# Kernel tuning notes

Measured on AMD Instinct MI355X. Metric: run time of the kernel, lower is better.

The kernel has to match this reference:

```python
import jax, jax.numpy as jnp
import numpy as np

SIGMA = 1.0


def _rbf_kernel(X, sigma):
    # pairwise squared Euclidean distances: ||xi||^2 + ||xj||^2 - 2 xi.xj
    sq = jnp.sum(X * X, axis=1)  # [n]
    d2 = sq[:, None] + sq[None, :] - 2.0 * (X @ X.T)
    d2 = jnp.maximum(d2, 0.0)
    return jnp.exp(-d2 / (2.0 * sigma ** 2))


def _center(K):
    # Kc = H @ K @ H with H = I - 11^T/n, done in O(n^2):
    # Kc = K - row_mean - col_mean + grand_mean
    row_mean = jnp.mean(K, axis=1, keepdims=True)   # [n,1]
    col_mean = jnp.mean(K, axis=0, keepdims=True)   # [1,n]
    grand = jnp.mean(K)
    return K - row_mean - col_mean + grand


def setup_inputs() -> dict:
    key = jax.random.key(0)
    k1, k2 = jax.random.split(key)
    X = jax.random.normal(k1, (8192, 512), dtype=jnp.float32)
    Y = jax.random.normal(k2, (8192, 512), dtype=jnp.float32)
    return {"X": X, "Y": Y}


def reference(X, Y):
    n = X.shape[0]
    K = _rbf_kernel(X, SIGMA)
    L = _rbf_kernel(Y, SIGMA)
    Kc = _center(K)
    Lc = _center(L)
    # trace(Kc @ Lc) == sum(Kc * Lc^T) == sum(Kc * Lc) since Lc symmetric
    hsic_value = jnp.sum(Kc * Lc) / (n - 1) ** 2
    return hsic_value
```

## Files before the change

### kernel.cpp

```cpp
#include <hip/hip_runtime.h>
#include <hip/hip_bf16.h>

#define N 8192
#define D 512
#define BM 128
#define BK 64

typedef __attribute__((ext_vector_type(4))) float f32x4;
typedef __attribute__((ext_vector_type(8))) short bf16x8;

__device__ __forceinline__ void g2l16(const void* g, void* l) {
  __builtin_amdgcn_global_load_lds(
      (const __attribute__((address_space(1))) void*)g,
      (__attribute__((address_space(3))) void*)l, 16, 0, 0);
}

__device__ __forceinline__ unsigned short f32_to_bf16(float f) {
  unsigned int u = __float_as_uint(f);
  unsigned int r = (u + 0x7fffu + ((u >> 16) & 1u)) >> 16;
  return (unsigned short)r;
}

__device__ __forceinline__ int lds_off(int row, int kobyte) {
  return row * BK + ((kobyte ^ ((row & 7) << 4)) >> 1);
}

__global__ __launch_bounds__(128) void prep_kernel(
    const float* __restrict__ X, const float* __restrict__ Y,
    unsigned short* __restrict__ Xb, unsigned short* __restrict__ Yb,
    float* __restrict__ sqX, float* __restrict__ sqY) {
  const int b = blockIdx.x;
  const int row = b & (N - 1);
  const float* src = (b < N) ? X : Y;
  unsigned short* dst = (b < N) ? Xb : Yb;
  float* sq = (b < N) ? sqX : sqY;
  const int t = threadIdx.x;
  float4 v = reinterpret_cast<const float4*>(src + (size_t)row * D)[t];
  unsigned short b0 = f32_to_bf16(v.x), b1 = f32_to_bf16(v.y),
                 b2 = f32_to_bf16(v.z), b3 = f32_to_bf16(v.w);
  float f0 = __uint_as_float((unsigned)b0 << 16);
  float f1 = __uint_as_float((unsigned)b1 << 16);
  float f2 = __uint_as_float((unsigned)b2 << 16);
  float f3 = __uint_as_float((unsigned)b3 << 16);
  float s = f0 * f0 + f1 * f1 + f2 * f2 + f3 * f3;
  ushort4 o; o.x = b0; o.y = b1; o.z = b2; o.w = b3;
  reinterpret_cast<ushort4*>(dst + (size_t)row * D)[t] = o;
  #pragma unroll
  for (int msk = 1; msk < 64; msk <<= 1) s += __shfl_xor(s, msk);
  __shared__ float red[2];
  if ((t & 63) == 0) red[t >> 6] = s;
  __syncthreads();
  if (t == 0) sq[row] = red[0] + red[1];
}

__global__ __launch_bounds__(256, 2) void hsic_main(
    const unsigned short* __restrict__ Xb, const unsigned short* __restrict__ Yb,
    const float* __restrict__ sqX, const float* __restrict__ sqY,
    float* __restrict__ rowK, float* __restrict__ rowL,
    float* __restrict__ sums) {
  __shared__ __align__(16) unsigned short sXi[BM * BK];
  __shared__ __align__(16) unsigned short sXj[BM * BK];
  __shared__ __align__(16) unsigned short sYi[BM * BK];
  __shared__ __align__(16) unsigned short sYj[BM * BK];

  const int bid = blockIdx.x;
  int ti = (int)((129.0f - sqrtf(16641.0f - 8.0f * (float)bid)) * 0.5f);
  while (ti > 0 && (ti * (129 - ti)) / 2 > bid) --ti;
  while (((ti + 1) * (128 - ti)) / 2 <= bid) ++ti;
  const int tj = ti + (bid - (ti * (129 - ti)) / 2);
  const bool diag = (ti == tj);

  const int ib = ti * BM, jb = tj * BM;
  const int t = threadIdx.x;
  const int lane = t & 63, wave = t >> 6;
  const int wr = wave >> 1, wc = wave & 1;
  const int fr = lane & 15, fq = lane >> 4;

  f32x4 accK[4][4], accL[4][4];
  #pragma unroll
  for (int m = 0; m < 4; ++m)
    #pragma unroll
    for (int n = 0; n < 4; ++n) { accK[m][n] = (f32x4)0.f; accL[m][n] = (f32x4)0.f; }

  const unsigned short* s0 = Xb + (size_t)ib * D;
  const unsigned short* s1 = Xb + (size_t)jb * D;
  const unsigned short* s2 = Yb + (size_t)ib * D;
  const unsigned short* s3 = Yb + (size_t)jb * D;

  const int srow = t >> 3;
  const int scb = (t & 7) * 16;
  const int swcb = scb ^ ((srow & 7) << 4);

  for (int kt = 0; kt < D / BK; ++kt) {
    const int kb = kt * BK;
    #pragma unroll
    for (int q = 0; q < 4; ++q) {
      const int row = q * 32 + srow;
      const size_t goff = (size_t)row * D + kb + (swcb >> 1);
      const int loff = q * 2048 + t * 8;
      g2l16(s0 + goff, sXi + loff);
      g2l16(s1 + goff, sXj + loff);
      g2l16(s2 + goff, sYi + loff);
      g2l16(s3 + goff, sYj + loff);
    }
    __syncthreads();
    #pragma unroll
    for (int kk = 0; kk < 2; ++kk) {
      const int kob = kk * 64 + fq * 16;
      bf16x8 a[4], b[4];
      #pragma unroll
      for (int m = 0; m < 4; ++m)
        a[m] = *(const bf16x8*)&sXi[lds_off(wr * 64 + m * 16 + fr, kob)];
      #pragma unroll
      for (int n = 0; n < 4; ++n)
        b[n] = *(const bf16x8*)&sXj[lds_off(wc * 64 + n * 16 + fr, kob)];
      #pragma unroll
      for (int m = 0; m < 4; ++m)
        #pragma unroll
        for (int n = 0; n < 4; ++n)
          accK[m][n] = __builtin_amdgcn_mfma_f32_16x16x32_bf16(a[m], b[n], accK[m][n], 0, 0, 0);
      #pragma unroll
      for (int m = 0; m < 4; ++m)
        a[m] = *(const bf16x8*)&sYi[lds_off(wr * 64 + m * 16 + fr, kob)];
      #pragma unroll
      for (int n = 0; n < 4; ++n)
        b[n] = *(const bf16x8*)&sYj[lds_off(wc * 64 + n * 16 + fr, kob)];
      #pragma unroll
      for (int m = 0; m < 4; ++m)
        #pragma unroll
        for (int n = 0; n < 4; ++n)
          accL[m][n] = __builtin_amdgcn_mfma_f32_16x16x32_bf16(a[m], b[n], accL[m][n], 0, 0, 0);
    }
    __syncthreads();
  }

  float sxj[4], syj[4];
  #pragma unroll
  for (int n = 0; n < 4; ++n) {
    const int j = jb + wc * 64 + n * 16 + fr;
    sxj[n] = sqX[j];
    syj[n] = sqY[j];
  }
  float kl = 0.f;
  float ckK[4] = {0.f, 0.f, 0.f, 0.f}, ckL[4] = {0.f, 0.f, 0.f, 0.f};
  #pragma unroll
  for (int m = 0; m < 4; ++m) {
    #pragma unroll
    for (int r = 0; r < 4; ++r) {
      const int i = ib + wr * 64 + m * 16 + fq * 4 + r;
      const float sxi = sqX[i], syi = sqY[i];
      float rk = 0.f, rl = 0.f;
      #pragma unroll
      for (int n = 0; n < 4; ++n) {
        float dK = fmaxf(sxi + sxj[n] - 2.f * accK[m][n][r], 0.f);
        float Kv = __expf(-0.5f * dK);
        float dL = fmaxf(syi + syj[n] - 2.f * accL[m][n][r], 0.f);
        float Lv = __expf(-0.5f * dL);
        kl += Kv * Lv;
        rk += Kv; rl += Lv;
        ckK[n] += Kv; ckL[n] += Lv;
      }
      #pragma unroll
      for (int msk = 1; msk < 16; msk <<= 1) {
        rk += __shfl_xor(rk, msk);
        rl += __shfl_xor(rl, msk);
      }
      if (fr == 0) {
        atomicAdd(&rowK[i], rk);
        atomicAdd(&rowL[i], rl);
      }
    }
  }
  if (!diag) {
    #pragma unroll
    for (int n = 0; n < 4; ++n) {
      float a = ckK[n], b = ckL[n];
      a += __shfl_xor(a, 16); a += __shfl_xor(a, 32);
      b += __shfl_xor(b, 16); b += __shfl_xor(b, 32);
      if (fq == 0) {
        const int j = jb + wc * 64 + n * 16 + fr;
        atomicAdd(&rowK[j], a);
        atomicAdd(&rowL[j], b);
      }
    }
    kl *= 2.f;
  }
  #pragma unroll
  for (int msk = 1; msk < 64; msk <<= 1) kl += __shfl_xor(kl, msk);
  __shared__ float klred[4];
  if (lane == 0) klred[wave] = kl;
  __syncthreads();
  if (t == 0) atomicAdd(sums, klred[0] + klred[1] + klred[2] + klred[3]);
}

__global__ __launch_bounds__(256) void finalize_kernel(
    const float* __restrict__ rowK, const float* __restrict__ rowL,
    const float* __restrict__ sums, float* __restrict__ out) {
  const int t = threadIdx.x;
  float dp = 0.f, sk = 0.f, sl = 0.f;
  for (int i = t; i < N; i += 256) {
    float a = rowK[i], b = rowL[i];
    dp += a * b; sk += a; sl += b;
  }
  #pragma unroll
  for (int msk = 1; msk < 64; msk <<= 1) {
    dp += __shfl_xor(dp, msk);
    sk += __shfl_xor(sk, msk);
    sl += __shfl_xor(sl, msk);
  }
  __shared__ float r[3][4];
  const int wave = t >> 6, lane = t & 63;
  if (lane == 0) { r[0][wave] = dp; r[1][wave] = sk; r[2][wave] = sl; }
  __syncthreads();
  if (t == 0) {
    float DP = r[0][0] + r[0][1] + r[0][2] + r[0][3];
    float SK = r[1][0] + r[1][1] + r[1][2] + r[1][3];
    float SL = r[2][0] + r[2][1] + r[2][2] + r[2][3];
    const float n = (float)N;
    float raw = sums[0] - (2.f / n) * DP + (SK / n) * (SL / n);
    out[0] = raw / ((n - 1.f) * (n - 1.f));
  }
}

extern "C" void kernel_launch(void* const* d_in, const int* in_sizes, int n_in,
                              void* d_out, int out_size, void* d_ws, size_t ws_size,
                              hipStream_t stream) {
  const float* X = (const float*)d_in[0];
  const float* Y = (const float*)d_in[1];
  char* ws = (char*)d_ws;
  unsigned short* Xb = (unsigned short*)ws;
  unsigned short* Yb = (unsigned short*)(ws + (size_t)N * D * 2);
  float* sqX = (float*)(ws + (size_t)N * D * 4);
  float* sqY = sqX + N;
  float* rowK = sqY + N;
  float* rowL = rowK + N;
  float* sums = rowL + N;

  hipMemsetAsync(rowK, 0, (size_t)(2 * N + 16) * sizeof(float), stream);
  prep_kernel<<<2 * N, 128, 0, stream>>>(X, Y, Xb, Yb, sqX, sqY);
  const int ntiles = (N / BM) * (N / BM + 1) / 2;
  hsic_main<<<ntiles, 256, 0, stream>>>(Xb, Yb, sqX, sqY, rowK, rowL, sums);
  finalize_kernel<<<1, 256, 0, stream>>>(rowK, rowL, sums, (float*)d_out);
}
```

Before: 187.7 us.

## Software-pipeline X/Y tile staging so global loads overlap MFMA compute

Splits each K-step into separate X and Y stages. Once an operand's fragments are in registers, the next K-tile for that operand is issued with async global-to-LDS loads, and the MFMAs run while those loads are in flight. Manual vmcnt/lgkmcnt waits and raw barriers replace the two __syncthreads per iteration, and s_setprio raises wave priority around the MFMA blocks. This hides global memory latency without adding LDS, but it holds twice as many fragment registers and relies on hand-counted wait counts being correct.

```diff
diff --git a/kernel.cpp b/kernel.cpp
--- a/kernel.cpp
+++ b/kernel.cpp
@@ -91,7 +91,7 @@
   const int scb = (t & 7) * 16;
   const int swcb = scb ^ ((srow & 7) << 4);
 
-  for (int kt = 0; kt < D / BK; ++kt) {
+  auto stageX = [&](int kt) {
     const int kb = kt * BK;
     #pragma unroll
     for (int q = 0; q < 4; ++q) {
@@ -100,39 +100,71 @@
       const int loff = q * 2048 + t * 8;
       g2l16(s0 + goff, sXi + loff);
       g2l16(s1 + goff, sXj + loff);
+    }
+  };
+  auto stageY = [&](int kt) {
+    const int kb = kt * BK;
+    #pragma unroll
+    for (int q = 0; q < 4; ++q) {
+      const int row = q * 32 + srow;
+      const size_t goff = (size_t)row * D + kb + (swcb >> 1);
+      const int loff = q * 2048 + t * 8;
       g2l16(s2 + goff, sYi + loff);
       g2l16(s3 + goff, sYj + loff);
     }
-    __syncthreads();
+  };
+
+  bf16x8 a[2][4], b[2][4];
+  auto loadFrags = [&](const unsigned short* si, const unsigned short* sj) {
     #pragma unroll
     for (int kk = 0; kk < 2; ++kk) {
       const int kob = kk * 64 + fq * 16;
-      bf16x8 a[4], b[4];
       #pragma unroll
       for (int m = 0; m < 4; ++m)
-        a[m] = *(const bf16x8*)&sXi[lds_off(wr * 64 + m * 16 + fr, kob)];
+        a[kk][m] = *(const bf16x8*)&si[lds_off(wr * 64 + m * 16 + fr, kob)];
       #pragma unroll
       for (int n = 0; n < 4; ++n)
-        b[n] = *(const bf16x8*)&sXj[lds_off(wc * 64 + n * 16 + fr, kob)];
+        b[kk][n] = *(const bf16x8*)&sj[lds_off(wc * 64 + n * 16 + fr, kob)];
+    }
+  };
+  auto mmaInto = [&](f32x4 (&acc)[4][4]) {
+    __builtin_amdgcn_s_setprio(1);
+    #pragma unroll
+    for (int kk = 0; kk < 2; ++kk)
       #pragma unroll
       for (int m = 0; m < 4; ++m)
         #pragma unroll
         for (int n = 0; n < 4; ++n)
-          accK[m][n] = __builtin_amdgcn_mfma_f32_16x16x32_bf16(a[m], b[n], accK[m][n], 0, 0, 0);
-      #pragma unroll
-      for (int m = 0; m < 4; ++m)
-        a[m] = *(const bf16x8*)&sYi[lds_off(wr * 64 + m * 16 + fr, kob)];
-      #pragma unroll
-      for (int n = 0; n < 4; ++n)
-        b[n] = *(const bf16x8*)&sYj[lds_off(wc * 64 + n * 16 + fr, kob)];
-      #pragma unroll
-      for (int m = 0; m < 4; ++m)
-        #pragma unroll
-        for (int n = 0; n < 4; ++n)
-          accL[m][n] = __builtin_amdgcn_mfma_f32_16x16x32_bf16(a[m], b[n], accL[m][n], 0, 0, 0);
-    }
-    __syncthreads();
-  }
+          acc[m][n] = __builtin_amdgcn_mfma_f32_16x16x32_bf16(a[kk][m], b[kk][n], acc[m][n], 0, 0, 0);
+    __builtin_amdgcn_s_setprio(0);
+  };
+
+  stageX(0);
+  stageY(0);
+  for (int kt = 0; kt < 7; ++kt) {
+    asm volatile("s_waitcnt vmcnt(8)" ::: "memory");
+    __builtin_amdgcn_s_barrier();
+    loadFrags(sXi, sXj);
+    asm volatile("s_waitcnt lgkmcnt(0)" ::: "memory");
+    __builtin_amdgcn_s_barrier();
+    stageX(kt + 1);
+    mmaInto(accK);
+    asm volatile("s_waitcnt vmcnt(8)" ::: "memory");
+    __builtin_amdgcn_s_barrier();
+    loadFrags(sYi, sYj);
+    asm volatile("s_waitcnt lgkmcnt(0)" ::: "memory");
+    __builtin_amdgcn_s_barrier();
+    stageY(kt + 1);
+    mmaInto(accL);
+  }
+  asm volatile("s_waitcnt vmcnt(8)" ::: "memory");
+  __builtin_amdgcn_s_barrier();
+  loadFrags(sXi, sXj);
+  mmaInto(accK);
+  asm volatile("s_waitcnt vmcnt(0)" ::: "memory");
+  __builtin_amdgcn_s_barrier();
+  loadFrags(sYi, sYj);
+  mmaInto(accL);
 
   float sxj[4], syj[4];
   #pragma unroll
@@ -174,13 +206,13 @@
   if (!diag) {
     #pragma unroll
     for (int n = 0; n < 4; ++n) {
-      float a = ckK[n], b = ckL[n];
-      a += __shfl_xor(a, 16); a += __shfl_xor(a, 32);
-      b += __shfl_xor(b, 16); b += __shfl_xor(b, 32);
+      float a2 = ckK[n], b2 = ckL[n];
+      a2 += __shfl_xor(a2, 16); a2 += __shfl_xor(a2, 32);
+      b2 += __shfl_xor(b2, 16); b2 += __shfl_xor(b2, 32);
       if (fq == 0) {
         const int j = jb + wc * 64 + n * 16 + fr;
-        atomicAdd(&rowK[j], a);
-        atomicAdd(&rowL[j], b);
+        atomicAdd(&rowK[j], a2);
+        atomicAdd(&rowL[j], b2);
       }
     }
     kl *= 2.f;
```

Result: faster. 175.9 us (-6.3%).

## Load MFMA operands directly from global memory, drop LDS staging, remap blocks for XCDs

Applied to the files above, without the earlier changes.

Removes the shared-memory tiles and barriers: each wave now loads its bf16 A/B fragments straight from global memory (relying on L1/L2 for reuse across waves) and issues the MFMAs, with s_setprio raised around the MFMA burst. The block index is permuted so consecutive tiles are spread across the 8 XCDs (blockIdx&7 chunks of 260), aiming to improve L2 locality. The occupancy hint in launch_bounds is dropped. This trades LDS traffic and sync cost for redundant global/cache loads, since each operand row is fetched by two waves with no LDS sharing, and there is no software prefetch to hide load latency.

```diff
diff --git a/kernel.cpp b/kernel.cpp
--- a/kernel.cpp
+++ b/kernel.cpp
@@ -4,25 +4,15 @@
 #define N 8192
 #define D 512
 #define BM 128
-#define BK 64
+#define NKT 16
 
 typedef __attribute__((ext_vector_type(4))) float f32x4;
 typedef __attribute__((ext_vector_type(8))) short bf16x8;
-
-__device__ __forceinline__ void g2l16(const void* g, void* l) {
-  __builtin_amdgcn_global_load_lds(
-      (const __attribute__((address_space(1))) void*)g,
-      (__attribute__((address_space(3))) void*)l, 16, 0, 0);
-}
 
 __device__ __forceinline__ unsigned short f32_to_bf16(float f) {
   unsigned int u = __float_as_uint(f);
   unsigned int r = (u + 0x7fffu + ((u >> 16) & 1u)) >> 16;
   return (unsigned short)r;
-}
-
-__device__ __forceinline__ int lds_off(int row, int kobyte) {
-  return row * BK + ((kobyte ^ ((row & 7) << 4)) >> 1);
 }
 
 __global__ __launch_bounds__(128) void prep_kernel(
@@ -53,17 +43,12 @@
   if (t == 0) sq[row] = red[0] + red[1];
 }
 
-__global__ __launch_bounds__(256, 2) void hsic_main(
+__global__ __launch_bounds__(256) void hsic_main(
     const unsigned short* __restrict__ Xb, const unsigned short* __restrict__ Yb,
     const float* __restrict__ sqX, const float* __restrict__ sqY,
     float* __restrict__ rowK, float* __restrict__ rowL,
     float* __restrict__ sums) {
-  __shared__ __align__(16) unsigned short sXi[BM * BK];
-  __shared__ __align__(16) unsigned short sXj[BM * BK];
-  __shared__ __align__(16) unsigned short sYi[BM * BK];
-  __shared__ __align__(16) unsigned short sYj[BM * BK];
-
-  const int bid = blockIdx.x;
+  const int bid = (blockIdx.x & 7) * 260 + (blockIdx.x >> 3);
   int ti = (int)((129.0f - sqrtf(16641.0f - 8.0f * (float)bid)) * 0.5f);
   while (ti > 0 && (ti * (129 - ti)) / 2 > bid) --ti;
   while (((ti + 1) * (128 - ti)) / 2 <= bid) ++ti;
@@ -82,56 +67,42 @@
     #pragma unroll
     for (int n = 0; n < 4; ++n) { accK[m][n] = (f32x4)0.f; accL[m][n] = (f32x4)0.f; }
 
-  const unsigned short* s0 = Xb + (size_t)ib * D;
-  const unsigned short* s1 = Xb + (size_t)jb * D;
-  const unsigned short* s2 = Yb + (size_t)ib * D;
-  const unsigned short* s3 = Yb + (size_t)jb * D;
-
-  const int srow = t >> 3;
-  const int scb = (t & 7) * 16;
-  const int swcb = scb ^ ((srow & 7) << 4);
-
-  for (int kt = 0; kt < D / BK; ++kt) {
-    const int kb = kt * BK;
-    #pragma unroll
-    for (int q = 0; q < 4; ++q) {
-      const int row = q * 32 + srow;
-      const size_t goff = (size_t)row * D + kb + (swcb >> 1);
-      const int loff = q * 2048 + t * 8;
-      g2l16(s0 + goff, sXi + loff);
-      g2l16(s1 + goff, sXj + loff);
-      g2l16(s2 + goff, sYi + loff);
-      g2l16(s3 + goff, sYj + loff);
-    }
-    __syncthreads();
-    #pragma unroll
-    for (int kk = 0; kk < 2; ++kk) {
-      const int kob = kk * 64 + fq * 16;
-      bf16x8 a[4], b[4];
-      #pragma unroll
-      for (int m = 0; m < 4; ++m)
-        a[m] = *(const bf16x8*)&sXi[lds_off(wr * 64 + m * 16 + fr, kob)];
+  int aoff[4], boff[4];
+  #pragma unroll
+  for (int m = 0; m < 4; ++m)
+    aoff[m] = (ib + wr * 64 + m * 16 + fr) * D + fq * 8;
+  #pragma unroll
+  for (int n = 0; n < 4; ++n)
+    boff[n] = (jb + wc * 64 + n * 16 + fr) * D + fq * 8;
+
+  #pragma unroll 1
+  for (int kt = 0; kt < NKT; ++kt) {
+    const int ko = kt * 32;
+    bf16x8 ax[4], bx[4], ay[4], by[4];
+    #pragma unroll
+    for (int m = 0; m < 4; ++m)
+      ax[m] = *(const bf16x8*)(Xb + aoff[m] + ko);
+    #pragma unroll
+    for (int n = 0; n < 4; ++n)
+      bx[n] = *(const bf16x8*)(Xb + boff[n] + ko);
+    #pragma unroll
+    for (int m = 0; m < 4; ++m)
+      ay[m] = *(const bf16x8*)(Yb + aoff[m] + ko);
+    #pragma unroll
+    for (int n = 0; n < 4; ++n)
+      by[n] = *(const bf16x8*)(Yb + boff[n] + ko);
+    __builtin_amdgcn_s_setprio(1);
+    #pragma unroll
+    for (int m = 0; m < 4; ++m)
       #pragma unroll
       for (int n = 0; n < 4; ++n)
-        b[n] = *(const bf16x8*)&sXj[lds_off(wc * 64 + n * 16 + fr, kob)];
-      #pragma unroll
-      for (int m = 0; m < 4; ++m)
-        #pragma unroll
-        for (int n = 0; n < 4; ++n)
-          accK[m][n] = __builtin_amdgcn_mfma_f32_16x16x32_bf16(a[m], b[n], accK[m][n], 0, 0, 0);
-      #pragma unroll
-      for (int m = 0; m < 4; ++m)
-        a[m] = *(const bf16x8*)&sYi[lds_off(wr * 64 + m * 16 + fr, kob)];
+        accK[m][n] = __builtin_amdgcn_mfma_f32_16x16x32_bf16(ax[m], bx[n], accK[m][n], 0, 0, 0);
+    #pragma unroll
+    for (int m = 0; m < 4; ++m)
       #pragma unroll
       for (int n = 0; n < 4; ++n)
-        b[n] = *(const bf16x8*)&sYj[lds_off(wc * 64 + n * 16 + fr, kob)];
-      #pragma unroll
-      for (int m = 0; m < 4; ++m)
-        #pragma unroll
-        for (int n = 0; n < 4; ++n)
-          accL[m][n] = __builtin_amdgcn_mfma_f32_16x16x32_bf16(a[m], b[n], accL[m][n], 0, 0, 0);
-    }
-    __syncthreads();
+        accL[m][n] = __builtin_amdgcn_mfma_f32_16x16x32_bf16(ay[m], by[n], accL[m][n], 0, 0, 0);
+    __builtin_amdgcn_s_setprio(0);
   }
 
   float sxj[4], syj[4];
@@ -174,13 +145,13 @@
   if (!diag) {
     #pragma unroll
     for (int n = 0; n < 4; ++n) {
-      float a = ckK[n], b = ckL[n];
-      a += __shfl_xor(a, 16); a += __shfl_xor(a, 32);
-      b += __shfl_xor(b, 16); b += __shfl_xor(b, 32);
+      float a2 = ckK[n], b2 = ckL[n];
+      a2 += __shfl_xor(a2, 16); a2 += __shfl_xor(a2, 32);
+      b2 += __shfl_xor(b2, 16); b2 += __shfl_xor(b2, 32);
       if (fq == 0) {
         const int j = jb + wc * 64 + n * 16 + fr;
-        atomicAdd(&rowK[j], a);
-        atomicAdd(&rowL[j], b);
+        atomicAdd(&rowK[j], a2);
+        atomicAdd(&rowL[j], b2);
       }
     }
     kl *= 2.f;
```

Measured after the change: 402.2 us. 114% more time.
